# Kernel optimization log

Measured on AMD Instinct MI355X. Metric: run time of the kernel, lower is better.

## Reference

```python
import jax, jax.numpy as jnp
import numpy as np

B, P, H, W, K = 2, 4096, 128, 128, 8
RADIUS = 0.05  # NDC-space point radius (raster_settings.radius)


def setup_inputs() -> dict:
    key = jax.random.key(0)
    k1, k2, k3 = jax.random.split(key, 3)
    points_world = jax.random.normal(k1, (B, P, 3), jnp.float32)
    # near-identity rotation (row-vector convention: X_view = X_world @ R + T)
    R = jnp.eye(3, dtype=jnp.float32)[None] + 0.01 * jax.random.normal(k2, (B, 3, 3), jnp.float32)
    # translate cloud to z ~ +3 so points are in front of the camera
    T = (0.1 * jax.random.normal(k3, (B, 3), jnp.float32)).at[:, 2].add(3.0)
    focal = jnp.full((B,), 1.5, jnp.float32)
    return {"points_world": points_world, "R": R, "T": T, "focal": focal}


def reference(points_world, R, T, focal):
    # --- camera transform: world -> view -> NDC (z kept in view space) ---
    pts_view = jnp.einsum('bpi,bij->bpj', points_world, R) + T[:, None, :]  # [B,P,3]
    z = pts_view[..., 2]                                                    # [B,P]
    x_ndc = focal[:, None] * pts_view[..., 0] / z
    y_ndc = focal[:, None] * pts_view[..., 1] / z

    # --- pixel-center NDC grid (pytorch3d convention: +x left, +y up) ---
    gx = 1.0 - 2.0 * (jnp.arange(W, dtype=jnp.float32) + 0.5) / W  # [W]
    gy = 1.0 - 2.0 * (jnp.arange(H, dtype=jnp.float32) + 0.5) / H  # [H]
    GY, GX = jnp.meshgrid(gy, gx, indexing='ij')
    gxf = GX.reshape(-1)  # [HW]
    gyf = GY.reshape(-1)

    # --- per-pixel candidate search: squared NDC distance to every point ---
    dist2 = (gxf[None, :, None] - x_ndc[:, None, :]) ** 2 \
          + (gyf[None, :, None] - y_ndc[:, None, :]) ** 2      # [B,HW,P]
    inside = (dist2 < RADIUS * RADIUS) & (z[:, None, :] > 0.0)  # in radius & in front

    # --- depth-sorted top-K nearest-in-z among covering points ---
    keyz = jnp.where(inside, z[:, None, :], jnp.inf)            # [B,HW,P]
    neg_top, idx_top = jax.lax.top_k(-keyz, K)                  # K smallest z
    zk = jnp.take_along_axis(keyz, idx_top, axis=-1)            # [B,HW,K]
    dk = jnp.take_along_axis(dist2, idx_top, axis=-1)
    valid = jnp.isfinite(zk)

    idx = jnp.where(valid, idx_top, -1).reshape(B, H, W, K)
    zbuf = jnp.where(valid, zk, -1.0).reshape(B, H, W, K)
    dists = jnp.where(valid, dk, -1.0).reshape(B, H, W, K)
    return idx, zbuf, dists
```

## Files before the change

kernel.cpp:

```cpp
#include <hip/hip_runtime.h>
#include <math.h>

#define BB 2
#define PP 4096
#define HH 128
#define WW 128
#define KK 8
#define TS 8
#define NTX (WW / TS)
#define NTY (HH / TS)
#define NW 8
#define SEG (PP / NW)
#define CIT (SEG / 64)
#define CAP 384

__global__ __launch_bounds__(64 * NW, 4) void raster_kernel(
    const float* __restrict__ pw,
    const float* __restrict__ Rm,
    const float* __restrict__ Tv,
    const float* __restrict__ fo,
    float* __restrict__ out,
    int N)
{
    __shared__ union {
        float4 cand[NW][CAP];
        struct { float z[NW][KK][64], i[NW][KK][64], d[NW][KK][64]; } mg;
    } sh;

    const int tx = blockIdx.x, ty = blockIdx.y, b = blockIdx.z;
    const int wv   = threadIdx.x >> 6;
    const int lane = threadIdx.x & 63;

    const float* r = Rm + b * 9;
    const float r00=r[0], r01=r[1], r02=r[2];
    const float r10=r[3], r11=r[4], r12=r[5];
    const float r20=r[6], r21=r[7], r22=r[8];
    const float t0=Tv[b*3+0], t1=Tv[b*3+1], t2=Tv[b*3+2];
    const float f = fo[b];

    const float R2f   = (float)(0.05 * 0.05);
    const float apron = 0.05f + 1e-5f;

    float gx_hi = 1.0f - 2.0f * ((float)(tx * TS)          + 0.5f) / (float)WW;
    float gx_lo = 1.0f - 2.0f * ((float)(tx * TS + TS - 1) + 0.5f) / (float)WW;
    float gy_hi = 1.0f - 2.0f * ((float)(ty * TS)          + 0.5f) / (float)HH;
    float gy_lo = 1.0f - 2.0f * ((float)(ty * TS + TS - 1) + 0.5f) / (float)HH;
    const float xmin = gx_lo - apron, xmax = gx_hi + apron;
    const float ymin = gy_lo - apron, ymax = gy_hi + apron;

    float px[CIT], py[CIT], pz[CIT];
    const float* basep = pw + ((size_t)b * PP + wv * SEG + lane) * 3;
#pragma unroll
    for (int it = 0; it < CIT; ++it) {
        px[it] = basep[it * 192 + 0];
        py[it] = basep[it * 192 + 1];
        pz[it] = basep[it * 192 + 2];
    }

    int cnt = 0;
#pragma unroll
    for (int it = 0; it < CIT; ++it) {
        int i = wv * SEG + it * 64 + lane;
        float x = px[it], y = py[it], z = pz[it];
        float vx = __fadd_rn(__fadd_rn(__fadd_rn(__fmul_rn(x, r00), __fmul_rn(y, r10)), __fmul_rn(z, r20)), t0);
        float vy = __fadd_rn(__fadd_rn(__fadd_rn(__fmul_rn(x, r01), __fmul_rn(y, r11)), __fmul_rn(z, r21)), t1);
        float vz = __fadd_rn(__fadd_rn(__fadd_rn(__fmul_rn(x, r02), __fmul_rn(y, r12)), __fmul_rn(z, r22)), t2);
        float xn = __fmul_rn(f, vx) / vz;
        float yn = __fmul_rn(f, vy) / vz;
        bool keep = (vz > 0.0f) && (xn >= xmin) && (xn <= xmax)
                                && (yn >= ymin) && (yn <= ymax);
        unsigned long long m = __ballot(keep);
        if (keep) {
            int slot = cnt + __popcll(m & ((1ull << lane) - 1ull));
            if (slot < CAP) sh.cand[wv][slot] = make_float4(xn, yn, vz, __int_as_float(i));
        }
        cnt += __popcll(m);
    }
    if (cnt > CAP) cnt = CAP;

    int w = tx * TS + (lane & (TS - 1));
    int h = ty * TS + (lane / TS);
    float gx = 1.0f - 2.0f * ((float)w + 0.5f) / (float)WW;
    float gy = 1.0f - 2.0f * ((float)h + 0.5f) / (float)HH;

    float zk[KK], dk[KK]; int ik[KK];
#pragma unroll
    for (int j = 0; j < KK; ++j) { zk[j] = INFINITY; dk[j] = -1.0f; ik[j] = -1; }

    for (int s = 0; s < cnt; ++s) {
        float4 q = sh.cand[wv][s];
        float dx = __fsub_rn(gx, q.x);
        float dy = __fsub_rn(gy, q.y);
        float d2 = __fadd_rn(__fmul_rn(dx, dx), __fmul_rn(dy, dy));
        float z = q.z;
        if (d2 < R2f && z < zk[KK - 1]) {
            int i = __float_as_int(q.w);
#pragma unroll
            for (int j = KK - 1; j >= 1; --j) {
                if (z < zk[j]) {
                    if (z < zk[j - 1]) { zk[j] = zk[j-1]; ik[j] = ik[j-1]; dk[j] = dk[j-1]; }
                    else               { zk[j] = z;       ik[j] = i;       dk[j] = d2;      }
                }
            }
            if (z < zk[0]) { zk[0] = z; ik[0] = i; dk[0] = d2; }
        }
    }

    __syncthreads();
#pragma unroll
    for (int s = 0; s < KK; ++s) {
        sh.mg.z[wv][s][lane] = zk[s];
        sh.mg.i[wv][s][lane] = __int_as_float(ik[s]);
        sh.mg.d[wv][s][lane] = dk[s];
    }
    __syncthreads();

    if (wv == 0) {
        float hz[NW], hd[NW]; int hi_[NW], hp[NW];
#pragma unroll
        for (int wq = 0; wq < NW; ++wq) {
            hp[wq]  = 0;
            hz[wq]  = sh.mg.z[wq][0][lane];
            hi_[wq] = __float_as_int(sh.mg.i[wq][0][lane]);
            hd[wq]  = sh.mg.d[wq][0][lane];
        }
        float A[KK], Z[KK], D[KK];
#pragma unroll
        for (int o = 0; o < KK; ++o) {
            int bw = 0;
#pragma unroll
            for (int wq = 1; wq < NW; ++wq) {
                bool better = (hz[wq] < hz[bw]) ||
                              ((hz[wq] == hz[bw]) && (hi_[wq] < hi_[bw]));
                if (better) bw = wq;
            }
            float sz = hz[0], sd = hd[0]; int si = hi_[0];
#pragma unroll
            for (int wq = 1; wq < NW; ++wq) {
                if (bw == wq) { sz = hz[wq]; sd = hd[wq]; si = hi_[wq]; }
            }
            A[o] = (float)si;
            Z[o] = (si >= 0) ? sz : -1.0f;
            D[o] = sd;
#pragma unroll
            for (int wq = 0; wq < NW; ++wq) {
                if (bw == wq) {
                    int p = ++hp[wq];
                    if (p < KK) {
                        hz[wq]  = sh.mg.z[wq][p][lane];
                        hi_[wq] = __float_as_int(sh.mg.i[wq][p][lane]);
                        hd[wq]  = sh.mg.d[wq][p][lane];
                    } else {
                        hz[wq] = INFINITY; hi_[wq] = -1; hd[wq] = -1.0f;
                    }
                }
            }
        }
        int pix  = (b * HH + h) * WW + w;
        int base = pix * KK;
        float4* oa = (float4*)(out + base);
        float4* oz = (float4*)(out + N + base);
        float4* od = (float4*)(out + 2 * N + base);
        oa[0] = ((float4*)A)[0]; oa[1] = ((float4*)A)[1];
        oz[0] = ((float4*)Z)[0]; oz[1] = ((float4*)Z)[1];
        od[0] = ((float4*)D)[0]; od[1] = ((float4*)D)[1];
    }
}

extern "C" void kernel_launch(void* const* d_in, const int* in_sizes, int n_in,
                              void* d_out, int out_size, void* d_ws, size_t ws_size,
                              hipStream_t stream) {
    const float* pw = (const float*)d_in[0];
    const float* Rm = (const float*)d_in[1];
    const float* Tv = (const float*)d_in[2];
    const float* fo = (const float*)d_in[3];
    int N = out_size / 3;

    hipLaunchKernelGGL(raster_kernel, dim3(NTX, NTY, BB), dim3(64 * NW), 0, stream,
                       pw, Rm, Tv, fo, (float*)d_out, N);
}
```

Measured before the change: 95.79 us.

## Split rasterizer into global point binning pass and per-tile top-K pass

Replaces the per-tile full scan of all points with a separate binning kernel that projects each point once and appends it via atomics to the bins of overlapping 8x8 tiles in workspace memory. The top-K kernel then loads only its tile's candidates and splits them across 4 waves instead of 8. Candidate order is now nondeterministic, so the insertion compare gains an index tie-break, and outputs use nontemporal stores. This removes the redundant per-tile projection of every point, but adds a memset, two extra launches and global atomics, and bins overflow silently past 512 entries.

Measured after the change: 102.0 us. 1.07x slower.

```diff
diff --git a/kernel.cpp b/kernel.cpp
--- a/kernel.cpp
+++ b/kernel.cpp
@@ -9,100 +9,119 @@
 #define TS 8
 #define NTX (WW / TS)
 #define NTY (HH / TS)
-#define NW 8
-#define SEG (PP / NW)
-#define CIT (SEG / 64)
-#define CAP 384
-
-__global__ __launch_bounds__(64 * NW, 4) void raster_kernel(
+#define NTILES (NTX * NTY)
+#define CAP2 512
+#define NW2 4
+
+typedef float vfloat4 __attribute__((ext_vector_type(4)));
+
+#define BIN_OFF 4096
+
+__global__ __launch_bounds__(256) void bin_kernel(
     const float* __restrict__ pw,
     const float* __restrict__ Rm,
     const float* __restrict__ Tv,
     const float* __restrict__ fo,
+    int* __restrict__ counters,
+    float4* __restrict__ bins)
+{
+    int t = blockIdx.x * blockDim.x + threadIdx.x;
+    if (t >= BB * PP) return;
+    int b = t >> 12;
+    int i = t & (PP - 1);
+
+    const float* r = Rm + b * 9;
+    const float* q = pw + (size_t)t * 3;
+    float x = q[0], y = q[1], z = q[2];
+    float vx = __fadd_rn(__fadd_rn(__fadd_rn(__fmul_rn(x, r[0]), __fmul_rn(y, r[3])), __fmul_rn(z, r[6])), Tv[b*3+0]);
+    float vy = __fadd_rn(__fadd_rn(__fadd_rn(__fmul_rn(x, r[1]), __fmul_rn(y, r[4])), __fmul_rn(z, r[7])), Tv[b*3+1]);
+    float vz = __fadd_rn(__fadd_rn(__fadd_rn(__fmul_rn(x, r[2]), __fmul_rn(y, r[5])), __fmul_rn(z, r[8])), Tv[b*3+2]);
+    float f = fo[b];
+    float xn = __fmul_rn(f, vx) / vz;
+    float yn = __fmul_rn(f, vy) / vz;
+
+    if (!(vz > 0.0f)) return;
+    if (fabsf(xn) > 1.2f || fabsf(yn) > 1.2f) return;
+
+    const float apron = 0.05f + 1e-5f;
+    float wpt = 64.0f * (1.0f - xn) - 0.5f;
+    float hpt = 64.0f * (1.0f - yn) - 0.5f;
+    int txlo = (int)floorf((wpt - 3.5f) / 8.0f), txhi = (int)floorf((wpt + 3.5f) / 8.0f);
+    int tylo = (int)floorf((hpt - 3.5f) / 8.0f), tyhi = (int)floorf((hpt + 3.5f) / 8.0f);
+    txlo = max(txlo, 0); txhi = min(txhi, NTX - 1);
+    tylo = max(tylo, 0); tyhi = min(tyhi, NTY - 1);
+
+    float4 rec = make_float4(xn, yn, vz, __int_as_float(i));
+    for (int ty = tylo; ty <= tyhi; ++ty) {
+        float gy_hi = 1.0f - 2.0f * ((float)(ty * TS)          + 0.5f) / (float)HH;
+        float gy_lo = 1.0f - 2.0f * ((float)(ty * TS + TS - 1) + 0.5f) / (float)HH;
+        if (!(yn >= gy_lo - apron && yn <= gy_hi + apron)) continue;
+        for (int tx = txlo; tx <= txhi; ++tx) {
+            float gx_hi = 1.0f - 2.0f * ((float)(tx * TS)          + 0.5f) / (float)WW;
+            float gx_lo = 1.0f - 2.0f * ((float)(tx * TS + TS - 1) + 0.5f) / (float)WW;
+            if (!(xn >= gx_lo - apron && xn <= gx_hi + apron)) continue;
+            int tid = b * NTILES + ty * NTX + tx;
+            int slot = atomicAdd(&counters[tid], 1);
+            if (slot < CAP2) bins[(size_t)tid * CAP2 + slot] = rec;
+        }
+    }
+}
+
+__global__ __launch_bounds__(64 * NW2) void topk_kernel(
+    const int* __restrict__ counters,
+    const float4* __restrict__ bins,
     float* __restrict__ out,
     int N)
 {
     __shared__ union {
-        float4 cand[NW][CAP];
-        struct { float z[NW][KK][64], i[NW][KK][64], d[NW][KK][64]; } mg;
+        float4 cand[CAP2];
+        struct { float z[NW2][KK][64], i[NW2][KK][64], d[NW2][KK][64]; } mg;
+        float pad[6144];
     } sh;
 
-    const int tx = blockIdx.x, ty = blockIdx.y, b = blockIdx.z;
+    const int tile = blockIdx.x, b = blockIdx.y;
+    const int tid  = b * NTILES + tile;
+    const int tx = tile & (NTX - 1), ty = tile >> 4;
     const int wv   = threadIdx.x >> 6;
     const int lane = threadIdx.x & 63;
 
-    const float* r = Rm + b * 9;
-    const float r00=r[0], r01=r[1], r02=r[2];
-    const float r10=r[3], r11=r[4], r12=r[5];
-    const float r20=r[6], r21=r[7], r22=r[8];
-    const float t0=Tv[b*3+0], t1=Tv[b*3+1], t2=Tv[b*3+2];
-    const float f = fo[b];
-
-    const float R2f   = (float)(0.05 * 0.05);
-    const float apron = 0.05f + 1e-5f;
-
-    float gx_hi = 1.0f - 2.0f * ((float)(tx * TS)          + 0.5f) / (float)WW;
-    float gx_lo = 1.0f - 2.0f * ((float)(tx * TS + TS - 1) + 0.5f) / (float)WW;
-    float gy_hi = 1.0f - 2.0f * ((float)(ty * TS)          + 0.5f) / (float)HH;
-    float gy_lo = 1.0f - 2.0f * ((float)(ty * TS + TS - 1) + 0.5f) / (float)HH;
-    const float xmin = gx_lo - apron, xmax = gx_hi + apron;
-    const float ymin = gy_lo - apron, ymax = gy_hi + apron;
-
-    float px[CIT], py[CIT], pz[CIT];
-    const float* basep = pw + ((size_t)b * PP + wv * SEG + lane) * 3;
-#pragma unroll
-    for (int it = 0; it < CIT; ++it) {
-        px[it] = basep[it * 192 + 0];
-        py[it] = basep[it * 192 + 1];
-        pz[it] = basep[it * 192 + 2];
-    }
-
-    int cnt = 0;
-#pragma unroll
-    for (int it = 0; it < CIT; ++it) {
-        int i = wv * SEG + it * 64 + lane;
-        float x = px[it], y = py[it], z = pz[it];
-        float vx = __fadd_rn(__fadd_rn(__fadd_rn(__fmul_rn(x, r00), __fmul_rn(y, r10)), __fmul_rn(z, r20)), t0);
-        float vy = __fadd_rn(__fadd_rn(__fadd_rn(__fmul_rn(x, r01), __fmul_rn(y, r11)), __fmul_rn(z, r21)), t1);
-        float vz = __fadd_rn(__fadd_rn(__fadd_rn(__fmul_rn(x, r02), __fmul_rn(y, r12)), __fmul_rn(z, r22)), t2);
-        float xn = __fmul_rn(f, vx) / vz;
-        float yn = __fmul_rn(f, vy) / vz;
-        bool keep = (vz > 0.0f) && (xn >= xmin) && (xn <= xmax)
-                                && (yn >= ymin) && (yn <= ymax);
-        unsigned long long m = __ballot(keep);
-        if (keep) {
-            int slot = cnt + __popcll(m & ((1ull << lane) - 1ull));
-            if (slot < CAP) sh.cand[wv][slot] = make_float4(xn, yn, vz, __int_as_float(i));
-        }
-        cnt += __popcll(m);
-    }
-    if (cnt > CAP) cnt = CAP;
+    int cnt = counters[tid];
+    if (cnt > CAP2) cnt = CAP2;
+
+    for (int s = threadIdx.x; s < cnt; s += 64 * NW2)
+        sh.cand[s] = bins[(size_t)tid * CAP2 + s];
+    __syncthreads();
 
     int w = tx * TS + (lane & (TS - 1));
     int h = ty * TS + (lane / TS);
     float gx = 1.0f - 2.0f * ((float)w + 0.5f) / (float)WW;
     float gy = 1.0f - 2.0f * ((float)h + 0.5f) / (float)HH;
+    const float R2f = (float)(0.05 * 0.05);
 
     float zk[KK], dk[KK]; int ik[KK];
 #pragma unroll
     for (int j = 0; j < KK; ++j) { zk[j] = INFINITY; dk[j] = -1.0f; ik[j] = -1; }
 
-    for (int s = 0; s < cnt; ++s) {
-        float4 q = sh.cand[wv][s];
+    for (int s = wv; s < cnt; s += NW2) {
+        float4 q = sh.cand[s];
         float dx = __fsub_rn(gx, q.x);
         float dy = __fsub_rn(gy, q.y);
         float d2 = __fadd_rn(__fmul_rn(dx, dx), __fmul_rn(dy, dy));
         float z = q.z;
-        if (d2 < R2f && z < zk[KK - 1]) {
-            int i = __float_as_int(q.w);
+        int   i = __float_as_int(q.w);
+        bool lessK = (z < zk[KK-1]) || (z == zk[KK-1] && i < ik[KK-1]);
+        if (d2 < R2f && lessK) {
 #pragma unroll
             for (int j = KK - 1; j >= 1; --j) {
-                if (z < zk[j]) {
-                    if (z < zk[j - 1]) { zk[j] = zk[j-1]; ik[j] = ik[j-1]; dk[j] = dk[j-1]; }
-                    else               { zk[j] = z;       ik[j] = i;       dk[j] = d2;      }
+                bool lj  = (z < zk[j])   || (z == zk[j]   && i < ik[j]);
+                bool ljm = (z < zk[j-1]) || (z == zk[j-1] && i < ik[j-1]);
+                if (lj) {
+                    if (ljm) { zk[j] = zk[j-1]; ik[j] = ik[j-1]; dk[j] = dk[j-1]; }
+                    else     { zk[j] = z;       ik[j] = i;       dk[j] = d2;      }
                 }
             }
-            if (z < zk[0]) { zk[0] = z; ik[0] = i; dk[0] = d2; }
+            bool l0 = (z < zk[0]) || (z == zk[0] && i < ik[0]);
+            if (l0) { zk[0] = z; ik[0] = i; dk[0] = d2; }
         }
     }
 
@@ -116,9 +135,9 @@
     __syncthreads();
 
     if (wv == 0) {
-        float hz[NW], hd[NW]; int hi_[NW], hp[NW];
-#pragma unroll
-        for (int wq = 0; wq < NW; ++wq) {
+        float hz[NW2], hd[NW2]; int hi_[NW2], hp[NW2];
+#pragma unroll
+        for (int wq = 0; wq < NW2; ++wq) {
             hp[wq]  = 0;
             hz[wq]  = sh.mg.z[wq][0][lane];
             hi_[wq] = __float_as_int(sh.mg.i[wq][0][lane]);
@@ -129,21 +148,21 @@
         for (int o = 0; o < KK; ++o) {
             int bw = 0;
 #pragma unroll
-            for (int wq = 1; wq < NW; ++wq) {
+            for (int wq = 1; wq < NW2; ++wq) {
                 bool better = (hz[wq] < hz[bw]) ||
                               ((hz[wq] == hz[bw]) && (hi_[wq] < hi_[bw]));
                 if (better) bw = wq;
             }
             float sz = hz[0], sd = hd[0]; int si = hi_[0];
 #pragma unroll
-            for (int wq = 1; wq < NW; ++wq) {
+            for (int wq = 1; wq < NW2; ++wq) {
                 if (bw == wq) { sz = hz[wq]; sd = hd[wq]; si = hi_[wq]; }
             }
             A[o] = (float)si;
             Z[o] = (si >= 0) ? sz : -1.0f;
             D[o] = sd;
 #pragma unroll
-            for (int wq = 0; wq < NW; ++wq) {
+            for (int wq = 0; wq < NW2; ++wq) {
                 if (bw == wq) {
                     int p = ++hp[wq];
                     if (p < KK) {
@@ -158,12 +177,15 @@
         }
         int pix  = (b * HH + h) * WW + w;
         int base = pix * KK;
-        float4* oa = (float4*)(out + base);
-        float4* oz = (float4*)(out + N + base);
-        float4* od = (float4*)(out + 2 * N + base);
-        oa[0] = ((float4*)A)[0]; oa[1] = ((float4*)A)[1];
-        oz[0] = ((float4*)Z)[0]; oz[1] = ((float4*)Z)[1];
-        od[0] = ((float4*)D)[0]; od[1] = ((float4*)D)[1];
+        vfloat4* oa = (vfloat4*)(out + base);
+        vfloat4* oz = (vfloat4*)(out + N + base);
+        vfloat4* od = (vfloat4*)(out + 2 * N + base);
+        __builtin_nontemporal_store(((vfloat4*)A)[0], oa);
+        __builtin_nontemporal_store(((vfloat4*)A)[1], oa + 1);
+        __builtin_nontemporal_store(((vfloat4*)Z)[0], oz);
+        __builtin_nontemporal_store(((vfloat4*)Z)[1], oz + 1);
+        __builtin_nontemporal_store(((vfloat4*)D)[0], od);
+        __builtin_nontemporal_store(((vfloat4*)D)[1], od + 1);
     }
 }
 
@@ -176,6 +198,12 @@
     const float* fo = (const float*)d_in[3];
     int N = out_size / 3;
 
-    hipLaunchKernelGGL(raster_kernel, dim3(NTX, NTY, BB), dim3(64 * NW), 0, stream,
-                       pw, Rm, Tv, fo, (float*)d_out, N);
+    int*    counters = (int*)d_ws;
+    float4* bins     = (float4*)((char*)d_ws + BIN_OFF);
+
+    (void)hipMemsetAsync(counters, 0, BB * NTILES * sizeof(int), stream);
+    hipLaunchKernelGGL(bin_kernel, dim3((BB * PP + 255) / 256), dim3(256), 0, stream,
+                       pw, Rm, Tv, fo, counters, bins);
+    hipLaunchKernelGGL(topk_kernel, dim3(NTILES, BB), dim3(64 * NW2), 0, stream,
+                       counters, bins, (float*)d_out, N);
 }
```
